# Performance work log

Measured on AMD Instinct MI355X. Metric: run time of the kernel, lower is better.

## Reference

```python
import jax, jax.numpy as jnp
import numpy as np

WINDOW = 34
WIN = WINDOW * 3 - 2  # 100, sliding window size


def _windowed_sum(a, w):
    # a: [B, T] -> sliding-window sums of length w: [B, T - w + 1]
    c = jnp.cumsum(a, axis=-1)
    c = jnp.pad(c, ((0, 0), (1, 0)))  # prepend zero so c[..., i] = sum(a[..., :i])
    return c[..., w:] - c[..., :-w]


def setup_inputs() -> dict:
    key = jax.random.key(0)
    x = jax.random.normal(key, (512, 2, 32768), dtype=jnp.float32)
    return {"x": x}


def reference(x):
    w = jnp.float32(WIN)
    x1 = x[:, 0, :]  # [B, T]
    x2 = x[:, 1, :]
    s1 = _windowed_sum(x1, WIN)
    s2 = _windowed_sum(x2, WIN)
    s11 = _windowed_sum(x1 * x1, WIN)
    s22 = _windowed_sum(x2 * x2, WIN)
    s12 = _windowed_sum(x1 * x2, WIN)
    # Pearson: sum((x1-m1)*(x2-m2)) / (sqrt(sum (x1-m1)^2) * sqrt(sum (x2-m2)^2))
    cov = s12 - s1 * s2 / w
    v1 = s11 - s1 * s1 / w
    v2 = s22 - s2 * s2 / w
    corr = cov / (jnp.sqrt(v1) * jnp.sqrt(v2))  # [B, N]
    # attention_generation: subtract batch mean, keep positive part
    avg = corr.mean(axis=0)                     # [N]
    r = corr - avg
    attentions = r * (r > 0).astype(r.dtype)
    return attentions  # original returns (attentions, None)
```

## Files before the change

kernel.cpp:

```cpp
#include <hip/hip_runtime.h>

#define LROW 32768
#define NROW 512
#define WIN 100
#define NC (LROW - WIN + 1)
#define NT1 256
#define T 16
#define CT (T * NT1)
#define NTILE ((NC + CT - 1) / CT)
#define G 4
#define RG (NROW / G)
#define SEG (CT + WIN - 1)
#define SEGP (SEG + 3 * (SEG >> 4) + 4)
#define N_TOT (NROW * NC)
#define N4 (N_TOT / 4)
#define RSPLIT 32
#define RCHUNK (NROW / RSPLIT)

__device__ __forceinline__ int pad3(int e) { return e + 3 * (e >> 4); }

__global__ __launch_bounds__(NT1, 4)
void swc_pass1(const float* __restrict__ x, float* __restrict__ out)
{
    __shared__ float lds1[SEGP];
    __shared__ float lds2[SEGP];

    const int tile = (int)blockIdx.x % NTILE;
    const int rg   = (int)blockIdx.x / NTILE;
    const int j0   = tile * CT;
    const int seglen = min(SEG, LROW - j0);
    const int ncols  = min(CT, NC - j0);
    const int tid  = (int)threadIdx.x;
    const int c0   = tid * T;
    const int pbase = 19 * tid;

    const int r0 = rg * G;
    for (int rr = 0; rr < G; ++rr) {
        const int r = r0 + rr;
        const float* __restrict__ p1 = x + ((size_t)(2 * r) + 0) * LROW + j0;
        const float* __restrict__ p2 = x + ((size_t)(2 * r) + 1) * LROW + j0;
        __syncthreads();
        const int nvec = seglen >> 2;
        for (int i = tid; i < nvec; i += NT1) {
            float4 v1 = ((const float4*)p1)[i];
            float4 v2 = ((const float4*)p2)[i];
            int b = 4 * i + 3 * (i >> 2);
            lds1[b + 0] = v1.x; lds1[b + 1] = v1.y; lds1[b + 2] = v1.z; lds1[b + 3] = v1.w;
            lds2[b + 0] = v2.x; lds2[b + 1] = v2.y; lds2[b + 2] = v2.z; lds2[b + 3] = v2.w;
        }
        for (int e = (nvec << 2) + tid; e < seglen; e += NT1) {
            lds1[pad3(e)] = p1[e];
            lds2[pad3(e)] = p2[e];
        }
        __syncthreads();

        float s1 = 0.f, s2 = 0.f, s11 = 0.f, s22 = 0.f, s12 = 0.f;
        #pragma unroll
        for (int k = 0; k < WIN; ++k) {
            float a = lds1[pbase + k + 3 * (k >> 4)];
            float b = lds2[pbase + k + 3 * (k >> 4)];
            s1 += a; s2 += b;
            s11 = fmaf(a, a, s11);
            s22 = fmaf(b, b, s22);
            s12 = fmaf(a, b, s12);
        }
        float* __restrict__ orow = out + (size_t)r * NC + j0;
        #pragma unroll
        for (int m = 0; m < T; ++m) {
            if (m > 0) {
                const int ko = m - 1;
                const int kn = m - 1 + WIN;
                float a_o = lds1[pbase + ko];
                float b_o = lds2[pbase + ko];
                float a_i = lds1[pbase + kn + 3 * (kn >> 4)];
                float b_i = lds2[pbase + kn + 3 * (kn >> 4)];
                s1 += a_i - a_o;
                s2 += b_i - b_o;
                s11 += fmaf(a_i, a_i, -(a_o * a_o));
                s22 += fmaf(b_i, b_i, -(b_o * b_o));
                s12 += fmaf(a_i, b_i, -(a_o * b_o));
            }
            const float invw = 1.0f / (float)WIN;
            float cov = fmaf(-(s1 * invw), s2, s12);
            float v1v = fmaf(-(s1 * invw), s1, s11);
            float v2v = fmaf(-(s2 * invw), s2, s22);
            float corr = cov * rsqrtf(v1v * v2v);
            if (c0 + m < ncols) orow[c0 + m] = corr;
        }
    }
}

__global__ __launch_bounds__(256)
void swc_reduce(const float* __restrict__ out, float* __restrict__ colsum)
{
    int col = (int)blockIdx.x * 256 + (int)threadIdx.x;
    if (col >= NC) return;
    const int r0 = (int)blockIdx.y * RCHUNK;
    float s = 0.f;
    #pragma unroll
    for (int i = 0; i < RCHUNK; ++i)
        s += out[(size_t)(r0 + i) * NC + col];
    atomicAdd(&colsum[col], s);
}

__global__ __launch_bounds__(256)
void swc_pass2(float* __restrict__ out, const float* __restrict__ colsum)
{
    const float inv = 1.0f / (float)NROW;
    int base = (int)blockIdx.x * 2048 + (int)threadIdx.x;
    #pragma unroll
    for (int v = 0; v < 8; ++v) {
        int i4 = base + v * 256;
        if (i4 < N4) {
            float4 o = ((float4*)out)[i4];
            int idx = i4 << 2;
            int row = (int)((unsigned)idx / (unsigned)NC);
            int col = idx - row * NC;
            int c1 = col + 1, c2 = col + 2, c3 = col + 3;
            if (c1 >= NC) c1 -= NC;
            if (c2 >= NC) c2 -= NC;
            if (c3 >= NC) c3 -= NC;
            o.x = fmaxf(o.x - colsum[col] * inv, 0.f);
            o.y = fmaxf(o.y - colsum[c1] * inv, 0.f);
            o.z = fmaxf(o.z - colsum[c2] * inv, 0.f);
            o.w = fmaxf(o.w - colsum[c3] * inv, 0.f);
            ((float4*)out)[i4] = o;
        }
    }
}

extern "C" void kernel_launch(void* const* d_in, const int* in_sizes, int n_in,
                              void* d_out, int out_size, void* d_ws, size_t ws_size,
                              hipStream_t stream) {
    const float* x = (const float*)d_in[0];
    float* out = (float*)d_out;
    float* colsum = (float*)d_ws;

    hipMemsetAsync(colsum, 0, NC * sizeof(float), stream);
    swc_pass1<<<dim3(NTILE * RG), dim3(NT1), 0, stream>>>(x, out);
    swc_reduce<<<dim3((NC + 255) / 256, RSPLIT), dim3(256), 0, stream>>>(out, colsum);
    swc_pass2<<<dim3((N4 + 2047) / 2048), dim3(256), 0, stream>>>(out, colsum);
}
```

Measured before the change: 296.1 us.

## Load sliding-window inputs straight from global memory and split column reduction

Pass1 no longer stages each row segment through shared memory with barriers. Each thread now reads its own 100+16 element window directly from global memory as float4 loads and keeps the head and tail values in registers for the sliding update. The tail tile is handled by a guarded template variant. The atomic column reduction is replaced, when workspace allows, by a two-stage partial-sum reduction. This removes the LDS traffic and the syncthreads overhead, at the cost of redundant global/L2 reads for overlapping windows, higher register pressure, and an extra kernel launch.

```diff
diff --git a/kernel.cpp b/kernel.cpp
--- a/kernel.cpp
+++ b/kernel.cpp
@@ -7,91 +7,120 @@
 #define NT1 256
 #define T 16
 #define CT (T * NT1)
-#define NTILE ((NC + CT - 1) / CT)
+#define NTILE 8
 #define G 4
 #define RG (NROW / G)
-#define SEG (CT + WIN - 1)
-#define SEGP (SEG + 3 * (SEG >> 4) + 4)
 #define N_TOT (NROW * NC)
 #define N4 (N_TOT / 4)
 #define RSPLIT 32
 #define RCHUNK (NROW / RSPLIT)
 
-__device__ __forceinline__ int pad3(int e) { return e + 3 * (e >> 4); }
+__device__ __forceinline__ float gc(const float4 v, int c) {
+    return c == 0 ? v.x : c == 1 ? v.y : c == 2 ? v.z : v.w;
+}
+
+template<bool GUARD>
+__device__ __forceinline__ void row_compute(
+    const float4* __restrict__ q1, const float4* __restrict__ q2,
+    float* __restrict__ orow, int c0, int ncols, int vmax)
+{
+    const float4 z4 = make_float4(0.f, 0.f, 0.f, 0.f);
+    float s1 = 0.f, s2 = 0.f, s11 = 0.f, s22 = 0.f, s12 = 0.f;
+    float4 ha[4], hb[4], ta[4], tb[4];
+    #pragma unroll
+    for (int v = 0; v < 4; ++v) { ha[v] = q1[v]; hb[v] = q2[v]; }
+    #pragma unroll
+    for (int v = 0; v < 4; ++v) {
+        ta[v] = (!GUARD || (25 + v) <= vmax) ? q1[25 + v] : z4;
+        tb[v] = (!GUARD || (25 + v) <= vmax) ? q2[25 + v] : z4;
+    }
+    #pragma unroll
+    for (int v = 0; v < 25; ++v) {
+        float4 a, b;
+        if (v < 4) { a = ha[v]; b = hb[v]; }
+        else       { a = q1[v]; b = q2[v]; }
+        s1 += a.x; s2 += b.x; s11 = fmaf(a.x, a.x, s11); s22 = fmaf(b.x, b.x, s22); s12 = fmaf(a.x, b.x, s12);
+        s1 += a.y; s2 += b.y; s11 = fmaf(a.y, a.y, s11); s22 = fmaf(b.y, b.y, s22); s12 = fmaf(a.y, b.y, s12);
+        s1 += a.z; s2 += b.z; s11 = fmaf(a.z, a.z, s11); s22 = fmaf(b.z, b.z, s22); s12 = fmaf(a.z, b.z, s12);
+        s1 += a.w; s2 += b.w; s11 = fmaf(a.w, a.w, s11); s22 = fmaf(b.w, b.w, s22); s12 = fmaf(a.w, b.w, s12);
+    }
+    const float invw = 1.0f / (float)WIN;
+    #pragma unroll
+    for (int m = 0; m < T; ++m) {
+        if (m > 0) {
+            const int e = m - 1;
+            float a_i = gc(ta[e >> 2], e & 3);
+            float b_i = gc(tb[e >> 2], e & 3);
+            float a_o = gc(ha[e >> 2], e & 3);
+            float b_o = gc(hb[e >> 2], e & 3);
+            s1 += a_i - a_o;
+            s2 += b_i - b_o;
+            s11 += fmaf(a_i, a_i, -(a_o * a_o));
+            s22 += fmaf(b_i, b_i, -(b_o * b_o));
+            s12 += fmaf(a_i, b_i, -(a_o * b_o));
+        }
+        float cov = fmaf(-(s1 * invw), s2, s12);
+        float v1v = fmaf(-(s1 * invw), s1, s11);
+        float v2v = fmaf(-(s2 * invw), s2, s22);
+        float corr = cov * rsqrtf(v1v * v2v);
+        if (!GUARD || (c0 + m < ncols)) orow[c0 + m] = corr;
+    }
+}
 
 __global__ __launch_bounds__(NT1, 4)
 void swc_pass1(const float* __restrict__ x, float* __restrict__ out)
 {
-    __shared__ float lds1[SEGP];
-    __shared__ float lds2[SEGP];
-
-    const int tile = (int)blockIdx.x % NTILE;
-    const int rg   = (int)blockIdx.x / NTILE;
+    const int tile = (int)blockIdx.x & (NTILE - 1);
+    const int rg   = (int)blockIdx.x >> 3;
     const int j0   = tile * CT;
-    const int seglen = min(SEG, LROW - j0);
-    const int ncols  = min(CT, NC - j0);
     const int tid  = (int)threadIdx.x;
     const int c0   = tid * T;
-    const int pbase = 19 * tid;
+    const bool tailtile = (tile == NTILE - 1);
+    const int ncols = tailtile ? (NC - j0) : CT;
+    if (c0 >= ncols) return;
+    const int vmax = ((LROW - j0 - 4) >> 2) - (tid << 2);
 
     const int r0 = rg * G;
     for (int rr = 0; rr < G; ++rr) {
         const int r = r0 + rr;
-        const float* __restrict__ p1 = x + ((size_t)(2 * r) + 0) * LROW + j0;
-        const float* __restrict__ p2 = x + ((size_t)(2 * r) + 1) * LROW + j0;
-        __syncthreads();
-        const int nvec = seglen >> 2;
-        for (int i = tid; i < nvec; i += NT1) {
-            float4 v1 = ((const float4*)p1)[i];
-            float4 v2 = ((const float4*)p2)[i];
-            int b = 4 * i + 3 * (i >> 2);
-            lds1[b + 0] = v1.x; lds1[b + 1] = v1.y; lds1[b + 2] = v1.z; lds1[b + 3] = v1.w;
-            lds2[b + 0] = v2.x; lds2[b + 1] = v2.y; lds2[b + 2] = v2.z; lds2[b + 3] = v2.w;
-        }
-        for (int e = (nvec << 2) + tid; e < seglen; e += NT1) {
-            lds1[pad3(e)] = p1[e];
-            lds2[pad3(e)] = p2[e];
-        }
-        __syncthreads();
-
-        float s1 = 0.f, s2 = 0.f, s11 = 0.f, s22 = 0.f, s12 = 0.f;
-        #pragma unroll
-        for (int k = 0; k < WIN; ++k) {
-            float a = lds1[pbase + k + 3 * (k >> 4)];
-            float b = lds2[pbase + k + 3 * (k >> 4)];
-            s1 += a; s2 += b;
-            s11 = fmaf(a, a, s11);
-            s22 = fmaf(b, b, s22);
-            s12 = fmaf(a, b, s12);
-        }
+        const float4* __restrict__ q1 =
+            (const float4*)(x + ((size_t)(2 * r) + 0) * LROW + j0) + (tid << 2);
+        const float4* __restrict__ q2 =
+            (const float4*)(x + ((size_t)(2 * r) + 1) * LROW + j0) + (tid << 2);
         float* __restrict__ orow = out + (size_t)r * NC + j0;
-        #pragma unroll
-        for (int m = 0; m < T; ++m) {
-            if (m > 0) {
-                const int ko = m - 1;
-                const int kn = m - 1 + WIN;
-                float a_o = lds1[pbase + ko];
-                float b_o = lds2[pbase + ko];
-                float a_i = lds1[pbase + kn + 3 * (kn >> 4)];
-                float b_i = lds2[pbase + kn + 3 * (kn >> 4)];
-                s1 += a_i - a_o;
-                s2 += b_i - b_o;
-                s11 += fmaf(a_i, a_i, -(a_o * a_o));
-                s22 += fmaf(b_i, b_i, -(b_o * b_o));
-                s12 += fmaf(a_i, b_i, -(a_o * b_o));
-            }
-            const float invw = 1.0f / (float)WIN;
-            float cov = fmaf(-(s1 * invw), s2, s12);
-            float v1v = fmaf(-(s1 * invw), s1, s11);
-            float v2v = fmaf(-(s2 * invw), s2, s22);
-            float corr = cov * rsqrtf(v1v * v2v);
-            if (c0 + m < ncols) orow[c0 + m] = corr;
-        }
+        if (tailtile) row_compute<true >(q1, q2, orow, c0, ncols, vmax);
+        else          row_compute<false>(q1, q2, orow, c0, ncols, vmax);
     }
 }
 
 __global__ __launch_bounds__(256)
-void swc_reduce(const float* __restrict__ out, float* __restrict__ colsum)
+void swc_red1(const float* __restrict__ out, float* __restrict__ partial)
+{
+    int col = (int)blockIdx.x * 256 + (int)threadIdx.x;
+    if (col >= NC) return;
+    const int k  = (int)blockIdx.y;
+    const int r0 = k * RCHUNK;
+    float s = 0.f;
+    #pragma unroll
+    for (int i = 0; i < RCHUNK; ++i)
+        s += out[(size_t)(r0 + i) * NC + col];
+    partial[(size_t)k * NC + col] = s;
+}
+
+__global__ __launch_bounds__(256)
+void swc_red2(const float* __restrict__ partial, float* __restrict__ colsum)
+{
+    int col = (int)blockIdx.x * 256 + (int)threadIdx.x;
+    if (col >= NC) return;
+    float s = 0.f;
+    #pragma unroll
+    for (int k = 0; k < RSPLIT; ++k)
+        s += partial[(size_t)k * NC + col];
+    colsum[col] = s;
+}
+
+__global__ __launch_bounds__(256)
+void swc_reduce_atomic(const float* __restrict__ out, float* __restrict__ colsum)
 {
     int col = (int)blockIdx.x * 256 + (int)threadIdx.x;
     if (col >= NC) return;
@@ -135,9 +164,16 @@
     const float* x = (const float*)d_in[0];
     float* out = (float*)d_out;
     float* colsum = (float*)d_ws;
+    float* partial = colsum + NC;
+    const size_t need = (size_t)(NC + (size_t)RSPLIT * NC) * sizeof(float);
 
     hipMemsetAsync(colsum, 0, NC * sizeof(float), stream);
     swc_pass1<<<dim3(NTILE * RG), dim3(NT1), 0, stream>>>(x, out);
-    swc_reduce<<<dim3((NC + 255) / 256, RSPLIT), dim3(256), 0, stream>>>(out, colsum);
+    if (ws_size >= need) {
+        swc_red1<<<dim3((NC + 255) / 256, RSPLIT), dim3(256), 0, stream>>>(out, partial);
+        swc_red2<<<dim3((NC + 255) / 256), dim3(256), 0, stream>>>(partial, colsum);
+    } else {
+        swc_reduce_atomic<<<dim3((NC + 255) / 256, RSPLIT), dim3(256), 0, stream>>>(out, colsum);
+    }
     swc_pass2<<<dim3((N4 + 2047) / 2048), dim3(256), 0, stream>>>(out, colsum);
 }
```

Measured after the change: 416.0 us. 1.4x slower.
